# Kernel tuning notes

Hardware: AMD Instinct MI355X
Metric: run time of the kernel (lower is better)

Reference implementation:

```python
import jax, jax.numpy as jnp
import numpy as np
from jax import lax

B, T, H, E, N, K = 1024, 64, 512, 200000, 50000, 2
LN_EPS = 1e-5


def _layernorm(x, w, b):
    m = jnp.mean(x, axis=-1, keepdims=True)
    v = jnp.mean((x - m) ** 2, axis=-1, keepdims=True)
    return (x - m) * lax.rsqrt(v + LN_EPS) * w + b


def setup_inputs() -> dict:
    key = jax.random.key(0)
    ks = jax.random.split(key, 12)
    s = 1.0 / np.sqrt(H)
    actions = jax.random.randint(ks[0], (B, T), 0, E, dtype=jnp.int32)
    # each graph stops at a random step in [T//2, T]; actions after that are -1 (stop)
    stop_len = jax.random.randint(ks[1], (B,), T // 2, T + 1, dtype=jnp.int32)
    actions = jnp.where(jnp.arange(T)[None, :] >= stop_len[:, None], -1, actions)
    return {
        "actions_seq": actions,
        "edge_tokens": jax.random.normal(ks[2], (E, H), dtype=jnp.float32),
        "stop_indices": jnp.full((B,), E, dtype=jnp.int32),  # never equals a real edge id
        "question_tokens": jax.random.normal(ks[3], (B, H), dtype=jnp.float32),
        "node_tokens": jax.random.normal(ks[4], (N, H), dtype=jnp.float32),
        "start_node_locals": jax.random.randint(ks[5], (B * K,), 0, N, dtype=jnp.int32),
        "start_ptr": (jnp.arange(B + 1, dtype=jnp.int32) * K),
        "w_ih": jax.random.normal(ks[6], (3 * H, H), dtype=jnp.float32) * s,
        "w_hh": jax.random.normal(ks[7], (3 * H, H), dtype=jnp.float32) * s,
        "b_ih": jax.random.normal(ks[8], (3 * H,), dtype=jnp.float32) * s,
        "b_hh": jax.random.normal(ks[9], (3 * H,), dtype=jnp.float32) * s,
        "ln_w": jnp.ones((H,), dtype=jnp.float32),
        "ln_b": jnp.zeros((H,), dtype=jnp.float32),
    }


def reference(actions_seq, edge_tokens, stop_indices, question_tokens, node_tokens,
              start_node_locals, start_ptr, w_ih, w_hh, b_ih, b_hh, ln_w, ln_b):
    num_graphs, num_steps = actions_seq.shape
    max_edge = edge_tokens.shape[0]

    # start state: segment-mean of selected node tokens per graph
    counts = start_ptr[1:] - start_ptr[:-1]  # [B]
    seg = jnp.repeat(jnp.arange(num_graphs), counts,
                     total_repeat_length=start_node_locals.shape[0])
    start_sum = jax.ops.segment_sum(node_tokens[start_node_locals], seg,
                                    num_segments=num_graphs)  # [B,H]
    denom = jnp.maximum(counts, 1).astype(start_sum.dtype)[:, None]
    start_state = start_sum / denom

    h0 = _layernorm(question_tokens + start_state, ln_w, ln_b)
    done0 = jnp.zeros((num_graphs,), dtype=bool)

    def step(carry, a):  # a: [B] actions at this step
        h, done = carry
        emb = _layernorm(h, ln_w, ln_b)  # emitted BEFORE the update, as in torch
        is_stop = (a == stop_indices) | (a < 0)
        active = (~done) & (~is_stop)
        idx = jnp.clip(a, 0, max_edge - 1)
        x = edge_tokens[idx]  # [B,H] gather (dropout p=0 -> identity)
        gi = x @ w_ih.T + b_ih  # [B,3H]
        gh = h @ w_hh.T + b_hh  # [B,3H]
        i_r, i_z, i_n = jnp.split(gi, 3, axis=-1)
        h_r, h_z, h_n = jnp.split(gh, 3, axis=-1)
        r = jax.nn.sigmoid(i_r + h_r)
        z = jax.nn.sigmoid(i_z + h_z)
        n = jnp.tanh(i_n + r * h_n)
        h_next = (1.0 - z) * n + z * h
        h = jnp.where(active[:, None], h_next, h)
        done = done | is_stop
        return (h, done), emb

    (_, _), embs = lax.scan(step, (h0, done0), actions_seq.T)  # embs: [T,B,H]
    return jnp.transpose(embs, (1, 0, 2))  # [B,T,H]
```

## Files before the change

### kernel.cpp

```cpp
#include <hip/hip_runtime.h>
#include <math.h>

#define NB 1024
#define NT 64
#define NH 512
#define NE 200000
#define LN_EPS 1e-5f

typedef __bf16 bf16;
typedef __attribute__((ext_vector_type(8))) __bf16 bf16x8;
typedef __attribute__((ext_vector_type(4))) float f32x4;

__device__ __forceinline__ void ln_stats(float sum, float sq, float& mean, float& rstd) {
#pragma unroll
  for (int o = 32; o > 0; o >>= 1) {
    sum += __shfl_down(sum, o);
    sq  += __shfl_down(sq, o);
  }
  __shared__ float red[8];
  const int wid = threadIdx.x >> 6;
  if ((threadIdx.x & 63) == 0) { red[wid * 2] = sum; red[wid * 2 + 1] = sq; }
  __syncthreads();
  if (threadIdx.x == 0) {
    const float ts = red[0] + red[2] + red[4] + red[6];
    const float tq = red[1] + red[3] + red[5] + red[7];
    const float m  = ts * (1.0f / NH);
    const float var = tq * (1.0f / NH) - m * m;
    red[0] = m;
    red[1] = rsqrtf(var + LN_EPS);
  }
  __syncthreads();
  mean = red[0];
  rstd = red[1];
}

__device__ __forceinline__ float sigmoid_f(float x) {
  return 1.0f / (1.0f + __expf(-x));
}
__device__ __forceinline__ float tanh_f(float x) {
  x = fminf(fmaxf(x, -15.0f), 15.0f);
  const float e = __expf(2.0f * x);
  return (e - 1.0f) / (e + 1.0f);
}

__global__ void active_kernel(const int* __restrict__ actions,
                              const int* __restrict__ stopidx,
                              int* __restrict__ act_mask) {
  const int b = blockIdx.x * blockDim.x + threadIdx.x;
  if (b >= NB) return;
  const int si = stopidx[b];
  bool done = false;
  for (int t = 0; t < NT; ++t) {
    const int a = actions[b * NT + t];
    const bool is_stop = (a == si) || (a < 0);
    act_mask[b * NT + t] = (!done && !is_stop) ? 1 : 0;
    done = done || is_stop;
  }
}

__global__ void wcvt_kernel(const float* __restrict__ wih,
                            const float* __restrict__ whh,
                            bf16* __restrict__ wihb, bf16* __restrict__ whhb) {
  const int i = (blockIdx.x * 256 + threadIdx.x) * 4;
  const float4 a = *(const float4*)&wih[i];
  const float4 b = *(const float4*)&whh[i];
  union { bf16 h[4]; uint2 u; } pa, pb;
  pa.h[0] = (bf16)a.x; pa.h[1] = (bf16)a.y; pa.h[2] = (bf16)a.z; pa.h[3] = (bf16)a.w;
  pb.h[0] = (bf16)b.x; pb.h[1] = (bf16)b.y; pb.h[2] = (bf16)b.z; pb.h[3] = (bf16)b.w;
  *(uint2*)&wihb[i] = pa.u;
  *(uint2*)&whhb[i] = pb.u;
}

__global__ void xall_kernel(const int* __restrict__ actions,
                            const float* __restrict__ edges,
                            bf16* __restrict__ xbf) {
  const int row = blockIdx.x;
  int a = actions[row];
  a = min(max(a, 0), NE - 1);
  const int i = threadIdx.x * 2;
  const float2 v = *(const float2*)&edges[(size_t)a * NH + i];
  union { bf16 h[2]; unsigned u; } p;
  p.h[0] = (bf16)v.x; p.h[1] = (bf16)v.y;
  *(unsigned*)&xbf[(size_t)row * NH + i] = p.u;
}

__global__ void h0_kernel(const float* __restrict__ q,
                          const float* __restrict__ nodes,
                          const int* __restrict__ locals,
                          const int* __restrict__ ptr,
                          const float* __restrict__ lnw,
                          const float* __restrict__ lnb,
                          float* __restrict__ h0, bf16* __restrict__ h0b) {
  const int b = blockIdx.x;
  const int i = threadIdx.x * 2;
  const int p0 = ptr[b], p1 = ptr[b + 1];
  const float denom = fmaxf((float)(p1 - p0), 1.0f);
  float s0 = 0.f, s1 = 0.f;
  for (int p = p0; p < p1; ++p) {
    const int node = locals[p];
    const float2 nv = *(const float2*)&nodes[(size_t)node * NH + i];
    s0 += nv.x; s1 += nv.y;
  }
  const float2 qv = *(const float2*)&q[(size_t)b * NH + i];
  const float v0 = qv.x + s0 / denom;
  const float v1 = qv.y + s1 / denom;
  float mean, rstd;
  ln_stats(v0 + v1, v0 * v0 + v1 * v1, mean, rstd);
  const float2 lw = *(const float2*)&lnw[i];
  const float2 lb = *(const float2*)&lnb[i];
  float2 o;
  o.x = (v0 - mean) * rstd * lw.x + lb.x;
  o.y = (v1 - mean) * rstd * lw.y + lb.y;
  *(float2*)&h0[(size_t)b * NH + i] = o;
  union { bf16 h[2]; unsigned u; } p;
  p.h[0] = (bf16)o.x; p.h[1] = (bf16)o.y;
  *(unsigned*)&h0b[(size_t)b * NH + i] = p.u;
}

#define BK 128
__global__ __launch_bounds__(512) void gates_kernel(
    const float* __restrict__ hs_t, float* __restrict__ hs_n,
    const bf16* __restrict__ hbf, bf16* __restrict__ hbf_n,
    const bf16* __restrict__ xbf,
    const bf16* __restrict__ wihb, const bf16* __restrict__ whhb,
    const float* __restrict__ b_ih, const float* __restrict__ b_hh,
    const int* __restrict__ act_mask, int t) {
  __shared__ bf16 Xs[64][BK + 8];
  __shared__ bf16 Hs[64][BK + 8];
  __shared__ bf16 Wi[96][BK + 8];
  __shared__ bf16 Wh[96][BK + 8];
  __shared__ int s_any;

  const int tid = threadIdx.x;
  const int c0 = blockIdx.x * 32;
  const int b0 = blockIdx.y * 64;

  if (tid == 0) s_any = 0;
  __syncthreads();
  if (tid < 64 && act_mask[(b0 + tid) * NT + t]) s_any = 1;
  __syncthreads();

  if (!s_any) {
    const int row = tid >> 3, c4 = (tid & 7) * 4;
    const size_t off = (size_t)(b0 + row) * NH + c0 + c4;
    const float4 v = *(const float4*)&hs_t[off];
    *(float4*)&hs_n[off] = v;
    union { bf16 h[4]; uint2 u; } p;
    p.h[0] = (bf16)v.x; p.h[1] = (bf16)v.y; p.h[2] = (bf16)v.z; p.h[3] = (bf16)v.w;
    *(uint2*)&hbf_n[off] = p.u;
    return;
  }

  const int wave = tid >> 6, lane = tid & 63;
  const int ln15 = lane & 15, q8 = (lane >> 4) * 8;
  const int wrow = (wave & 3) * 16;
  const int nt = wave >> 2;

  f32x4 aR = {0, 0, 0, 0}, aZ = {0, 0, 0, 0}, aNI = {0, 0, 0, 0}, aNH = {0, 0, 0, 0};

  for (int kb = 0; kb < NH; kb += BK) {
    if (kb) __syncthreads();
#pragma unroll
    for (int i = 0; i < 2; ++i) {
      const int idx = tid + 512 * i;
      const int row = idx >> 4, c8 = (idx & 15) * 8;
      *(int4*)&Hs[row][c8] = *(const int4*)&hbf[(size_t)(b0 + row) * NH + kb + c8];
      *(int4*)&Xs[row][c8] =
          *(const int4*)&xbf[((size_t)(b0 + row) * NT + t) * NH + kb + c8];
    }
#pragma unroll
    for (int i = 0; i < 3; ++i) {
      const int idx = tid + 512 * i;
      const int row = idx >> 4, c8 = (idx & 15) * 8;
      const int g = row >> 5, n = row & 31;
      const size_t gr = ((size_t)g * NH + c0 + n) * NH + kb + c8;
      *(int4*)&Wi[row][c8] = *(const int4*)&wihb[gr];
      *(int4*)&Wh[row][c8] = *(const int4*)&whhb[gr];
    }
    __syncthreads();
#pragma unroll
    for (int k = 0; k < BK; k += 32) {
      const bf16x8 ax = *(const bf16x8*)&Xs[wrow + ln15][k + q8];
      const bf16x8 ah = *(const bf16x8*)&Hs[wrow + ln15][k + q8];
      const int wr = nt * 16 + ln15;
      const bf16x8 biR = *(const bf16x8*)&Wi[wr][k + q8];
      const bf16x8 bhR = *(const bf16x8*)&Wh[wr][k + q8];
      const bf16x8 biZ = *(const bf16x8*)&Wi[32 + wr][k + q8];
      const bf16x8 bhZ = *(const bf16x8*)&Wh[32 + wr][k + q8];
      const bf16x8 biN = *(const bf16x8*)&Wi[64 + wr][k + q8];
      const bf16x8 bhN = *(const bf16x8*)&Wh[64 + wr][k + q8];
      aR = __builtin_amdgcn_mfma_f32_16x16x32_bf16(ax, biR, aR, 0, 0, 0);
      aR = __builtin_amdgcn_mfma_f32_16x16x32_bf16(ah, bhR, aR, 0, 0, 0);
      aZ = __builtin_amdgcn_mfma_f32_16x16x32_bf16(ax, biZ, aZ, 0, 0, 0);
      aZ = __builtin_amdgcn_mfma_f32_16x16x32_bf16(ah, bhZ, aZ, 0, 0, 0);
      aNI = __builtin_amdgcn_mfma_f32_16x16x32_bf16(ax, biN, aNI, 0, 0, 0);
      aNH = __builtin_amdgcn_mfma_f32_16x16x32_bf16(ah, bhN, aNH, 0, 0, 0);
    }
  }

  const int c = c0 + nt * 16 + ln15;
  const float bR = b_ih[c] + b_hh[c];
  const float bZ = b_ih[NH + c] + b_hh[NH + c];
  const float bI = b_ih[2 * NH + c];
  const float bH = b_hh[2 * NH + c];
  const int mbase = b0 + wrow + (lane >> 4) * 4;
#pragma unroll
  for (int i = 0; i < 4; ++i) {
    const int m = mbase + i;
    const int act = act_mask[m * NT + t];
    const float hp = hs_t[(size_t)m * NH + c];
    const float r = sigmoid_f(aR[i] + bR);
    const float z = sigmoid_f(aZ[i] + bZ);
    const float n = tanh_f(aNI[i] + bI + r * (aNH[i] + bH));
    const float o = act ? ((1.0f - z) * n + z * hp) : hp;
    hs_n[(size_t)m * NH + c] = o;
    hbf_n[(size_t)m * NH + c] = (bf16)o;
  }
}

__global__ void ln_all_kernel(const float* __restrict__ hs,
                              const float* __restrict__ lnw,
                              const float* __restrict__ lnb,
                              float* __restrict__ out) {
  const int r = blockIdx.x;
  const int t = r >> 10, b = r & (NB - 1);
  const int i = threadIdx.x * 2;
  const float2 hv = *(const float2*)&hs[(size_t)r * NH + i];
  float mean, rstd;
  ln_stats(hv.x + hv.y, hv.x * hv.x + hv.y * hv.y, mean, rstd);
  const float2 lw = *(const float2*)&lnw[i];
  const float2 lb = *(const float2*)&lnb[i];
  float2 o;
  o.x = (hv.x - mean) * rstd * lw.x + lb.x;
  o.y = (hv.y - mean) * rstd * lw.y + lb.y;
  *(float2*)&out[((size_t)b * NT + t) * NH + i] = o;
}

extern "C" void kernel_launch(void* const* d_in, const int* in_sizes, int n_in,
                              void* d_out, int out_size, void* d_ws, size_t ws_size,
                              hipStream_t stream) {
  const int*   actions      = (const int*)d_in[0];
  const float* edge_tokens  = (const float*)d_in[1];
  const int*   stop_indices = (const int*)d_in[2];
  const float* question     = (const float*)d_in[3];
  const float* node_tokens  = (const float*)d_in[4];
  const int*   start_locals = (const int*)d_in[5];
  const int*   start_ptr    = (const int*)d_in[6];
  const float* w_ih         = (const float*)d_in[7];
  const float* w_hh         = (const float*)d_in[8];
  const float* b_ih         = (const float*)d_in[9];
  const float* b_hh         = (const float*)d_in[10];
  const float* ln_w         = (const float*)d_in[11];
  const float* ln_b         = (const float*)d_in[12];
  float* out = (float*)d_out;

  bf16* Wihbf = (bf16*)d_ws;
  bf16* Whhbf = Wihbf + (size_t)3 * NH * NH;
  bf16* Xbf   = Whhbf + (size_t)3 * NH * NH;
  float* hstates = (float*)(Xbf + (size_t)NB * NT * NH);
  bf16* Hb0 = (bf16*)(hstates + (size_t)NT * NB * NH);
  bf16* Hb1 = Hb0 + (size_t)NB * NH;
  int* act_mask = (int*)(Hb1 + (size_t)NB * NH);

  active_kernel<<<NB / 256, 256, 0, stream>>>(actions, stop_indices, act_mask);
  wcvt_kernel<<<(3 * NH * NH) / (256 * 4), 256, 0, stream>>>(w_ih, w_hh, Wihbf, Whhbf);
  xall_kernel<<<NB * NT, 256, 0, stream>>>(actions, edge_tokens, Xbf);
  h0_kernel<<<NB, 256, 0, stream>>>(question, node_tokens, start_locals, start_ptr,
                                    ln_w, ln_b, hstates, Hb0);

  bf16* hbc = Hb0;
  bf16* hbn = Hb1;
  for (int t = 0; t < NT - 1; ++t) {
    gates_kernel<<<dim3(NH / 32, NB / 64), 512, 0, stream>>>(
        hstates + (size_t)t * NB * NH, hstates + (size_t)(t + 1) * NB * NH,
        hbc, hbn, Xbf, Wihbf, Whhbf, b_ih, b_hh, act_mask, t);
    bf16* tmp = hbc; hbc = hbn; hbn = tmp;
  }

  ln_all_kernel<<<NB * NT, 256, 0, stream>>>(hstates, ln_w, ln_b, out);
}
```

Baseline: 1.404 ms.

## Hoist input-gate GEMM out of the recurrence into one batched GEMM

Computes x@W_ih^T for all timesteps up front in a single large tiled MFMA GEMM (gi_kernel) that writes fp32 gate preactivations to a workspace buffer. The per-step kernel then only does h@W_hh^T with a larger K tile and adds the precomputed input gates. This removes half of the serial per-step matmul work and raises utilisation for the input projection. In exchange it writes and re-reads a 64K x 1536 fp32 buffer (~400MB), computes gates for masked-out steps too, and needs extra workspace.

```diff
diff --git a/kernel.cpp b/kernel.cpp
--- a/kernel.cpp
+++ b/kernel.cpp
@@ -5,6 +5,8 @@
 #define NT 64
 #define NH 512
 #define NE 200000
+#define NG (3 * NH)
+#define MALL (NB * NT)
 #define LN_EPS 1e-5f
 
 typedef __bf16 bf16;
@@ -117,17 +119,70 @@
   *(unsigned*)&h0b[(size_t)b * NH + i] = p.u;
 }
 
-#define BK 128
-__global__ __launch_bounds__(512) void gates_kernel(
+#define GI_BK 64
+__global__ __launch_bounds__(512) void gi_kernel(const bf16* __restrict__ xbf,
+                                                 const bf16* __restrict__ wihb,
+                                                 float* __restrict__ gi) {
+  __shared__ bf16 As[128][GI_BK + 8];
+  __shared__ bf16 Bs[128][GI_BK + 8];
+  const int tid = threadIdx.x;
+  const int n0 = blockIdx.x * 128;
+  const size_t m0 = (size_t)blockIdx.y * 128;
+  const int wave = tid >> 6, lane = tid & 63;
+  const int ln15 = lane & 15, q8 = (lane >> 4) * 8;
+  const int wm = wave >> 2;
+  const int wn = wave & 3;
+
+  f32x4 acc[4][2] = {};
+
+  for (int kb = 0; kb < NH; kb += GI_BK) {
+    if (kb) __syncthreads();
+#pragma unroll
+    for (int i = 0; i < 2; ++i) {
+      const int idx = tid + 512 * i;
+      const int row = idx >> 3, c8 = (idx & 7) * 8;
+      *(int4*)&As[row][c8] = *(const int4*)&xbf[(m0 + row) * NH + kb + c8];
+      *(int4*)&Bs[row][c8] = *(const int4*)&wihb[(size_t)(n0 + row) * NH + kb + c8];
+    }
+    __syncthreads();
+#pragma unroll
+    for (int k = 0; k < GI_BK; k += 32) {
+      bf16x8 a[4], b[2];
+#pragma unroll
+      for (int mf = 0; mf < 4; ++mf)
+        a[mf] = *(const bf16x8*)&As[wm * 64 + mf * 16 + ln15][k + q8];
+#pragma unroll
+      for (int nf = 0; nf < 2; ++nf)
+        b[nf] = *(const bf16x8*)&Bs[wn * 32 + nf * 16 + ln15][k + q8];
+#pragma unroll
+      for (int mf = 0; mf < 4; ++mf)
+#pragma unroll
+        for (int nf = 0; nf < 2; ++nf)
+          acc[mf][nf] =
+              __builtin_amdgcn_mfma_f32_16x16x32_bf16(a[mf], b[nf], acc[mf][nf], 0, 0, 0);
+    }
+  }
+
+  const int q4 = (lane >> 4) * 4;
+#pragma unroll
+  for (int mf = 0; mf < 4; ++mf)
+#pragma unroll
+    for (int i = 0; i < 4; ++i) {
+      const size_t m = m0 + wm * 64 + mf * 16 + q4 + i;
+#pragma unroll
+      for (int nf = 0; nf < 2; ++nf)
+        gi[m * NG + n0 + wn * 32 + nf * 16 + ln15] = acc[mf][nf][i];
+    }
+}
+
+#define BK 256
+__global__ __launch_bounds__(512) void gh_kernel(
     const float* __restrict__ hs_t, float* __restrict__ hs_n,
     const bf16* __restrict__ hbf, bf16* __restrict__ hbf_n,
-    const bf16* __restrict__ xbf,
-    const bf16* __restrict__ wihb, const bf16* __restrict__ whhb,
+    const float* __restrict__ gi, const bf16* __restrict__ whhb,
     const float* __restrict__ b_ih, const float* __restrict__ b_hh,
     const int* __restrict__ act_mask, int t) {
-  __shared__ bf16 Xs[64][BK + 8];
   __shared__ bf16 Hs[64][BK + 8];
-  __shared__ bf16 Wi[96][BK + 8];
   __shared__ bf16 Wh[96][BK + 8];
   __shared__ int s_any;
 
@@ -156,63 +211,63 @@
   const int wrow = (wave & 3) * 16;
   const int nt = wave >> 2;
 
-  f32x4 aR = {0, 0, 0, 0}, aZ = {0, 0, 0, 0}, aNI = {0, 0, 0, 0}, aNH = {0, 0, 0, 0};
-
-  for (int kb = 0; kb < NH; kb += BK) {
-    if (kb) __syncthreads();
-#pragma unroll
-    for (int i = 0; i < 2; ++i) {
-      const int idx = tid + 512 * i;
-      const int row = idx >> 4, c8 = (idx & 15) * 8;
-      *(int4*)&Hs[row][c8] = *(const int4*)&hbf[(size_t)(b0 + row) * NH + kb + c8];
-      *(int4*)&Xs[row][c8] =
-          *(const int4*)&xbf[((size_t)(b0 + row) * NT + t) * NH + kb + c8];
-    }
-#pragma unroll
-    for (int i = 0; i < 3; ++i) {
-      const int idx = tid + 512 * i;
-      const int row = idx >> 4, c8 = (idx & 15) * 8;
-      const int g = row >> 5, n = row & 31;
-      const size_t gr = ((size_t)g * NH + c0 + n) * NH + kb + c8;
-      *(int4*)&Wi[row][c8] = *(const int4*)&wihb[gr];
-      *(int4*)&Wh[row][c8] = *(const int4*)&whhb[gr];
-    }
-    __syncthreads();
-#pragma unroll
-    for (int k = 0; k < BK; k += 32) {
-      const bf16x8 ax = *(const bf16x8*)&Xs[wrow + ln15][k + q8];
-      const bf16x8 ah = *(const bf16x8*)&Hs[wrow + ln15][k + q8];
-      const int wr = nt * 16 + ln15;
-      const bf16x8 biR = *(const bf16x8*)&Wi[wr][k + q8];
-      const bf16x8 bhR = *(const bf16x8*)&Wh[wr][k + q8];
-      const bf16x8 biZ = *(const bf16x8*)&Wi[32 + wr][k + q8];
-      const bf16x8 bhZ = *(const bf16x8*)&Wh[32 + wr][k + q8];
-      const bf16x8 biN = *(const bf16x8*)&Wi[64 + wr][k + q8];
-      const bf16x8 bhN = *(const bf16x8*)&Wh[64 + wr][k + q8];
-      aR = __builtin_amdgcn_mfma_f32_16x16x32_bf16(ax, biR, aR, 0, 0, 0);
-      aR = __builtin_amdgcn_mfma_f32_16x16x32_bf16(ah, bhR, aR, 0, 0, 0);
-      aZ = __builtin_amdgcn_mfma_f32_16x16x32_bf16(ax, biZ, aZ, 0, 0, 0);
-      aZ = __builtin_amdgcn_mfma_f32_16x16x32_bf16(ah, bhZ, aZ, 0, 0, 0);
-      aNI = __builtin_amdgcn_mfma_f32_16x16x32_bf16(ax, biN, aNI, 0, 0, 0);
-      aNH = __builtin_amdgcn_mfma_f32_16x16x32_bf16(ah, bhN, aNH, 0, 0, 0);
-    }
-  }
-
   const int c = c0 + nt * 16 + ln15;
   const float bR = b_ih[c] + b_hh[c];
   const float bZ = b_ih[NH + c] + b_hh[NH + c];
   const float bI = b_ih[2 * NH + c];
   const float bH = b_hh[2 * NH + c];
   const int mbase = b0 + wrow + (lane >> 4) * 4;
+  float giR[4], giZ[4], giN[4], hp[4];
+  int actv[4];
 #pragma unroll
   for (int i = 0; i < 4; ++i) {
     const int m = mbase + i;
-    const int act = act_mask[m * NT + t];
-    const float hp = hs_t[(size_t)m * NH + c];
-    const float r = sigmoid_f(aR[i] + bR);
-    const float z = sigmoid_f(aZ[i] + bZ);
-    const float n = tanh_f(aNI[i] + bI + r * (aNH[i] + bH));
-    const float o = act ? ((1.0f - z) * n + z * hp) : hp;
+    const size_t gr = ((size_t)m * NT + t) * NG;
+    giR[i] = gi[gr + c];
+    giZ[i] = gi[gr + NH + c];
+    giN[i] = gi[gr + 2 * NH + c];
+    hp[i]  = hs_t[(size_t)m * NH + c];
+    actv[i] = act_mask[m * NT + t];
+  }
+
+  f32x4 aR = {0, 0, 0, 0}, aZ = {0, 0, 0, 0}, aN = {0, 0, 0, 0};
+
+  for (int kb = 0; kb < NH; kb += BK) {
+    if (kb) __syncthreads();
+#pragma unroll
+    for (int i = 0; i < 4; ++i) {
+      const int idx = tid + 512 * i;
+      const int row = idx >> 5, c8 = (idx & 31) * 8;
+      *(int4*)&Hs[row][c8] = *(const int4*)&hbf[(size_t)(b0 + row) * NH + kb + c8];
+    }
+#pragma unroll
+    for (int i = 0; i < 6; ++i) {
+      const int idx = tid + 512 * i;
+      const int row = idx >> 5, c8 = (idx & 31) * 8;
+      const int g = row >> 5, n = row & 31;
+      *(int4*)&Wh[row][c8] = *(const int4*)&whhb[((size_t)g * NH + c0 + n) * NH + kb + c8];
+    }
+    __syncthreads();
+#pragma unroll
+    for (int k = 0; k < BK; k += 32) {
+      const bf16x8 ah = *(const bf16x8*)&Hs[wrow + ln15][k + q8];
+      const int wr = nt * 16 + ln15;
+      const bf16x8 bhR = *(const bf16x8*)&Wh[wr][k + q8];
+      const bf16x8 bhZ = *(const bf16x8*)&Wh[32 + wr][k + q8];
+      const bf16x8 bhN = *(const bf16x8*)&Wh[64 + wr][k + q8];
+      aR = __builtin_amdgcn_mfma_f32_16x16x32_bf16(ah, bhR, aR, 0, 0, 0);
+      aZ = __builtin_amdgcn_mfma_f32_16x16x32_bf16(ah, bhZ, aZ, 0, 0, 0);
+      aN = __builtin_amdgcn_mfma_f32_16x16x32_bf16(ah, bhN, aN, 0, 0, 0);
+    }
+  }
+
+#pragma unroll
+  for (int i = 0; i < 4; ++i) {
+    const int m = mbase + i;
+    const float r = sigmoid_f(aR[i] + giR[i] + bR);
+    const float z = sigmoid_f(aZ[i] + giZ[i] + bZ);
+    const float n = tanh_f(giN[i] + bI + r * (aN[i] + bH));
+    const float o = actv[i] ? ((1.0f - z) * n + z * hp[i]) : hp[i];
     hs_n[(size_t)m * NH + c] = o;
     hbf_n[(size_t)m * NH + c] = (bf16)o;
   }
@@ -257,7 +312,8 @@
   bf16* Wihbf = (bf16*)d_ws;
   bf16* Whhbf = Wihbf + (size_t)3 * NH * NH;
   bf16* Xbf   = Whhbf + (size_t)3 * NH * NH;
-  float* hstates = (float*)(Xbf + (size_t)NB * NT * NH);
+  float* GI   = (float*)(Xbf + (size_t)MALL * NH);
+  float* hstates = GI + (size_t)MALL * NG;
   bf16* Hb0 = (bf16*)(hstates + (size_t)NT * NB * NH);
   bf16* Hb1 = Hb0 + (size_t)NB * NH;
   int* act_mask = (int*)(Hb1 + (size_t)NB * NH);
@@ -268,12 +324,14 @@
   h0_kernel<<<NB, 256, 0, stream>>>(question, node_tokens, start_locals, start_ptr,
                                     ln_w, ln_b, hstates, Hb0);
 
+  gi_kernel<<<dim3(NG / 128, MALL / 128), 512, 0, stream>>>(Xbf, Wihbf, GI);
+
   bf16* hbc = Hb0;
   bf16* hbn = Hb1;
   for (int t = 0; t < NT - 1; ++t) {
-    gates_kernel<<<dim3(NH / 32, NB / 64), 512, 0, stream>>>(
+    gh_kernel<<<dim3(NH / 32, NB / 64), 512, 0, stream>>>(
         hstates + (size_t)t * NB * NH, hstates + (size_t)(t + 1) * NB * NH,
-        hbc, hbn, Xbf, Wihbf, Whhbf, b_ih, b_hh, act_mask, t);
+        hbc, hbn, GI, Whhbf, b_ih, b_hh, act_mask, t);
     bf16* tmp = hbc; hbc = hbn; hbn = tmp;
   }
 
```

Measured after the change: 1.491 ms. 6.2% more time.
